# Performance work log

Hardware: AMD Instinct MI355X
Metric: run time of the kernel (lower is better)

## Reference

```python
import jax, jax.numpy as jnp
from jax import lax
import numpy as np

B, N, C = 8, 16384, 128
NPOINT, NSAMPLE = 1024, 64
RADIUS = 0.3
MLP = [C + 3, 64, 64, 128]  # use_xyz adds 3 input channels


def furthest_point_sample(xyz, npoint):
    """xyz: (B, N, 3) -> inds: (B, npoint) int32, iterative FPS starting at index 0."""
    b, n, _ = xyz.shape
    init_idx = jnp.zeros((b,), jnp.int32)
    mind0 = jnp.full((b, n), 1e10, xyz.dtype)

    def step(carry, _):
        mind, last = carry
        p = jnp.take_along_axis(xyz, last[:, None, None], axis=1)  # (B,1,3)
        d = jnp.sum((xyz - p) ** 2, axis=-1)                       # (B,N)
        mind = jnp.minimum(mind, d)
        nxt = jnp.argmax(mind, axis=-1).astype(jnp.int32)
        return (mind, nxt), nxt

    (_, _), rest = lax.scan(step, (mind0, init_idx), None, length=npoint - 1)
    return jnp.concatenate([init_idx[None], rest], axis=0).T  # (B, npoint)


def ball_query(xyz, new_xyz, radius, nsample):
    """Return (B, npoint, nsample) indices: first nsample points within radius of
    each center; slots past the found count are filled with the first in-ball index
    (matches CUDA ball_query semantics)."""
    n = xyz.shape[1]
    d2 = jnp.sum((new_xyz[:, :, None, :] - xyz[:, None, :, :]) ** 2, axis=-1)  # (B,npoint,N)
    mask = d2 < radius * radius
    score = jnp.where(mask, -jnp.arange(n, dtype=jnp.int32), jnp.int32(-n))
    top, _ = lax.top_k(score, nsample)            # largest scores = smallest valid indices
    idx = -top
    valid = top > -n
    return jnp.where(valid, idx, idx[..., :1])    # pad with first in-ball index


def gather_points(x, idx):
    """x: (B, N, D) or (B, D, N) gathered per batch along point axis via vmap."""
    if x.ndim == 3 and x.shape[-1] != idx.shape[-1]:
        pass
    return x


def reference(xyz, features, W0, b0, W1, b1, W2, b2):
    inds = furthest_point_sample(xyz, NPOINT)                               # (B,npoint)
    new_xyz = jax.vmap(lambda p, i: p[i])(xyz, inds)                        # (B,npoint,3)

    idx = ball_query(xyz, new_xyz, RADIUS, NSAMPLE)                         # (B,npoint,nsample)
    grouped_xyz = jax.vmap(lambda p, i: p[i])(xyz, idx)                     # (B,npoint,nsample,3)
    grouped_xyz = grouped_xyz - new_xyz[:, :, None, :]                      # center-relative
    gx = jnp.transpose(grouped_xyz, (0, 3, 1, 2))                           # (B,3,npoint,nsample)
    gf = jax.vmap(lambda f, i: f[:, i])(features, idx)                      # (B,C,npoint,nsample)
    x = jnp.concatenate([gx, gf], axis=1)                                   # (B,C+3,npoint,nsample)

    # SharedMLP: pointwise Conv2d (1x1) + ReLU per layer
    for W, b in ((W0, b0), (W1, b1), (W2, b2)):
        x = jax.nn.relu(jnp.einsum('bcps,oc->bops', x, W) + b[None, :, None, None])

    new_features = jnp.max(x, axis=-1)                                      # max pool over nsample
    return new_xyz, new_features, inds


def setup_inputs() -> dict:
    key = jax.random.key(0)
    ks = jax.random.split(key, 8)
    inp = {
        'xyz': jax.random.normal(ks[0], (B, N, 3), jnp.float32),
        'features': jax.random.normal(ks[1], (B, C, N), jnp.float32),
    }
    for i in range(3):
        cin, cout = MLP[i], MLP[i + 1]
        inp[f'W{i}'] = jax.random.normal(ks[2 + 2 * i], (cout, cin), jnp.float32) * 0.05
        inp[f'b{i}'] = jax.random.normal(ks[3 + 2 * i], (cout,), jnp.float32) * 0.01
    return inp
```

## Files before the change

kernel.cpp:

```cpp
#include <hip/hip_runtime.h>

#define BATCH   8
#define NPTS    16384
#define NCH     128
#define NPOINT  1024
#define NSAMPLE 64
#define CIN     131

#define THREADS  1024
#define FPS_PPT  (NPTS / THREADS)
#define CTAG     0x7C000000u

typedef unsigned long long u64;

__device__ __forceinline__ u64 u64max(u64 a, u64 b) { return a > b ? a : b; }

__device__ __forceinline__ u64 shfl_xor_u64(u64 v, int off) {
  const unsigned lo = __shfl_xor((unsigned)v, off, 64);
  const unsigned hi = __shfl_xor((unsigned)(v >> 32), off, 64);
  return ((u64)hi << 32) | lo;
}

__global__ void wtrans_kernel(const float* __restrict__ W0,
                              const float* __restrict__ W1,
                              const float* __restrict__ W2,
                              float* __restrict__ w0t,
                              float* __restrict__ w1t,
                              float* __restrict__ w2t)
{
  const int t = blockIdx.x * blockDim.x + threadIdx.x;
  if (t < 64 * CIN) { const int oc = t / CIN, ic = t % CIN; w0t[ic * 64  + oc] = W0[t]; }
  if (t < 64 * 64)  { const int oc = t >> 6,  ic = t & 63;  w1t[ic * 64  + oc] = W1[t]; }
  if (t < 128 * 64) { const int oc = t / 64,  ic = t % 64;  w2t[ic * 128 + oc] = W2[t]; }
}

__global__ __launch_bounds__(THREADS) void mega_kernel(
    const float* __restrict__ xyz, const float* __restrict__ feat,
    const float* __restrict__ w0t, const float* __restrict__ b0,
    const float* __restrict__ w1t, const float* __restrict__ b1,
    const float* __restrict__ w2t, const float* __restrict__ b2,
    float* __restrict__ out_newxyz, float* __restrict__ out_feat,
    float* __restrict__ out_inds_f, u64* __restrict__ cslot)
{
  __shared__ float sA[CIN * 64];
  __shared__ float sB[64 * 64];
  __shared__ int   s_idx[NSAMPLE];
  __shared__ int   bq[4][NSAMPLE];
  __shared__ int   bqcnt[4], bqfirst[4];
  __shared__ u64   s_w[2][16];
  __shared__ unsigned s_sel[4];

  const int t = threadIdx.x;

  if (blockIdx.x < BATCH) {
    const int b = blockIdx.x;
    const int lane = t & 63, wid = t >> 6;
    const float* __restrict__ p = xyz + (size_t)b * NPTS * 3;

    float xs[FPS_PPT], ys[FPS_PPT], zs[FPS_PPT], mind[FPS_PPT];
#pragma unroll
    for (int i = 0; i < FPS_PPT; ++i) {
      const int n = t + i * THREADS;
      xs[i] = p[n * 3 + 0];
      ys[i] = p[n * 3 + 1];
      zs[i] = p[n * 3 + 2];
      mind[i] = 1e10f;
    }

    u64* __restrict__ cs = cslot + (size_t)b * NPOINT * 4;

    float px = p[0], py = p[1], pz = p[2];
    if (t == 0) {
      out_inds_f[b * NPOINT] = 0.0f;
      const size_t o = (size_t)b * NPOINT * 3;
      out_newxyz[o + 0] = px; out_newxyz[o + 1] = py; out_newxyz[o + 2] = pz;
      const u64 tg = (u64)CTAG << 32;
      __hip_atomic_store(&cs[1], tg | __float_as_uint(px), __ATOMIC_RELAXED, __HIP_MEMORY_SCOPE_AGENT);
      __hip_atomic_store(&cs[2], tg | __float_as_uint(py), __ATOMIC_RELAXED, __HIP_MEMORY_SCOPE_AGENT);
      __hip_atomic_store(&cs[3], tg | __float_as_uint(pz), __ATOMIC_RELAXED, __HIP_MEMORY_SCOPE_AGENT);
      __hip_atomic_store(&cs[0], tg | 0u, __ATOMIC_RELAXED, __HIP_MEMORY_SCOPE_AGENT);
    }

    for (int k = 1; k < NPOINT; ++k) {
      const int par = k & 1;

      float bestv = -1.0f;
      int   besti = 0;
#pragma unroll
      for (int i = 0; i < FPS_PPT; ++i) {
        const float dx = xs[i] - px;
        const float dy = ys[i] - py;
        const float dz = zs[i] - pz;
        const float d = __fadd_rn(__fadd_rn(__fmul_rn(dx, dx), __fmul_rn(dy, dy)),
                                  __fmul_rn(dz, dz));
        const float m = fminf(mind[i], d);
        mind[i] = m;
        if (m > bestv) { bestv = m; besti = t + i * THREADS; }
      }

      u64 pk = ((u64)__float_as_uint(bestv) << 18) | (u64)(besti ^ 0x3FFFF);
#pragma unroll
      for (int off = 32; off >= 1; off >>= 1) pk = u64max(pk, shfl_xor_u64(pk, off));
      if (lane == 0) s_w[par][wid] = pk;
      __syncthreads();

      u64 bw = s_w[par][0];
#pragma unroll
      for (int i = 1; i < 16; ++i) bw = u64max(bw, s_w[par][i]);
      const int bi = (int)((~bw) & 0x3FFFF);

      px = p[bi * 3 + 0]; py = p[bi * 3 + 1]; pz = p[bi * 3 + 2];

      if (t == 0) {
        out_inds_f[b * NPOINT + k] = (float)bi;
        const size_t o = ((size_t)b * NPOINT + k) * 3;
        out_newxyz[o + 0] = px; out_newxyz[o + 1] = py; out_newxyz[o + 2] = pz;
        const u64 tg = (u64)(CTAG | (unsigned)k) << 32;
        u64* __restrict__ ck = cs + (size_t)k * 4;
        __hip_atomic_store(&ck[1], tg | __float_as_uint(px), __ATOMIC_RELAXED, __HIP_MEMORY_SCOPE_AGENT);
        __hip_atomic_store(&ck[2], tg | __float_as_uint(py), __ATOMIC_RELAXED, __HIP_MEMORY_SCOPE_AGENT);
        __hip_atomic_store(&ck[3], tg | __float_as_uint(pz), __ATOMIC_RELAXED, __HIP_MEMORY_SCOPE_AGENT);
        __hip_atomic_store(&ck[0], tg | (unsigned)bi, __ATOMIC_RELAXED, __HIP_MEMORY_SCOPE_AGENT);
      }
    }
    return;
  }

  const int c  = blockIdx.x - BATCH;
  const int b = c & 7, pc = c >> 3;
  const u64* __restrict__ cs = cslot + ((size_t)b * NPOINT + pc) * 4;

  if (t < 4) {
    const unsigned tg = CTAG | (unsigned)pc;
    u64 v;
    for (;;) {
      v = __hip_atomic_load(cs + t, __ATOMIC_RELAXED, __HIP_MEMORY_SCOPE_AGENT);
      if ((unsigned)(v >> 32) == tg) break;
      __builtin_amdgcn_s_sleep(8);
    }
    s_sel[t] = (unsigned)v;
  }
  __syncthreads();
  const float cx = __uint_as_float(s_sel[1]);
  const float cy = __uint_as_float(s_sel[2]);
  const float cz = __uint_as_float(s_sel[3]);
  const float* __restrict__ pb = xyz + (size_t)b * NPTS * 3;

  if (t < 256) {
    const int w = t >> 6, lane = t & 63;
    const float R2 = (float)(0.3 * 0.3);
    const int beg = w * (NPTS / 4);
    int cnt = 0, first = -1;
    for (int bs = beg; bs < beg + NPTS / 4; bs += 64) {
      const int n = bs + lane;
      const float dx = pb[n * 3 + 0] - cx;
      const float dy = pb[n * 3 + 1] - cy;
      const float dz = pb[n * 3 + 2] - cz;
      const float d = __fadd_rn(__fadd_rn(__fmul_rn(dx, dx), __fmul_rn(dy, dy)),
                                __fmul_rn(dz, dz));
      const bool in = d < R2;
      const u64 m = __ballot(in);
      if (first < 0 && m) first = bs + __ffsll(m) - 1;
      const int pos = __popcll(m & ((1ull << lane) - 1ull));
      if (in && cnt + pos < NSAMPLE) bq[w][cnt + pos] = n;
      cnt += __popcll(m);
      if (cnt >= NSAMPLE) break;
    }
    if (lane == 0) { bqcnt[w] = cnt < NSAMPLE ? cnt : NSAMPLE; bqfirst[w] = first; }
  }
  __syncthreads();
  if (t < NSAMPLE) {
    int firstAll = -1;
#pragma unroll
    for (int w = 0; w < 4; ++w)
      if (firstAll < 0 && bqfirst[w] >= 0) firstAll = bqfirst[w];
    int o = 0, val = -1;
#pragma unroll
    for (int w = 0; w < 4; ++w) {
      const int cw = bqcnt[w];
      if (val < 0 && t >= o && t < o + cw) val = bq[w][t - o];
      o += cw;
    }
    s_idx[t] = (val >= 0) ? val : firstAll;
  }
  __syncthreads();

  const int sm = t & 63, cg = t >> 6;
  const int is = s_idx[sm];
  if (cg == 0) {
    sA[0 * 64 + sm] = pb[is * 3 + 0] - cx;
    sA[1 * 64 + sm] = pb[is * 3 + 1] - cy;
    sA[2 * 64 + sm] = pb[is * 3 + 2] - cz;
  }
  const float* __restrict__ fb = feat + (size_t)b * NCH * NPTS;
  for (int ch = cg; ch < NCH; ch += 16)
    sA[(3 + ch) * 64 + sm] = fb[(size_t)ch * NPTS + is];
  __syncthreads();

  const int s0  = (t & 15) * 4;
  const int oc0 = ((t >> 4) & 15) * 4;

  if (t < 256) {
    float acc[4][4];
#pragma unroll
    for (int j = 0; j < 4; ++j) {
      const float bj = b0[oc0 + j];
#pragma unroll
      for (int i = 0; i < 4; ++i) acc[i][j] = bj;
    }
    for (int ic = 0; ic < CIN; ++ic) {
      const float4 xv = *(const float4*)&sA[ic * 64 + s0];
      const float4 wv = *(const float4*)&w0t[ic * 64 + oc0];
      const float xr[4] = {xv.x, xv.y, xv.z, xv.w};
      const float wr[4] = {wv.x, wv.y, wv.z, wv.w};
#pragma unroll
      for (int i = 0; i < 4; ++i)
#pragma unroll
        for (int j = 0; j < 4; ++j) acc[i][j] += xr[i] * wr[j];
    }
#pragma unroll
    for (int j = 0; j < 4; ++j) {
      float4 r;
      r.x = fmaxf(acc[0][j], 0.f); r.y = fmaxf(acc[1][j], 0.f);
      r.z = fmaxf(acc[2][j], 0.f); r.w = fmaxf(acc[3][j], 0.f);
      *(float4*)&sB[(oc0 + j) * 64 + s0] = r;
    }
  }
  __syncthreads();

  if (t < 256) {
    float acc[4][4];
#pragma unroll
    for (int j = 0; j < 4; ++j) {
      const float bj = b1[oc0 + j];
#pragma unroll
      for (int i = 0; i < 4; ++i) acc[i][j] = bj;
    }
    for (int ic = 0; ic < 64; ++ic) {
      const float4 xv = *(const float4*)&sB[ic * 64 + s0];
      const float4 wv = *(const float4*)&w1t[ic * 64 + oc0];
      const float xr[4] = {xv.x, xv.y, xv.z, xv.w};
      const float wr[4] = {wv.x, wv.y, wv.z, wv.w};
#pragma unroll
      for (int i = 0; i < 4; ++i)
#pragma unroll
        for (int j = 0; j < 4; ++j) acc[i][j] += xr[i] * wr[j];
    }
#pragma unroll
    for (int j = 0; j < 4; ++j) {
      float4 r;
      r.x = fmaxf(acc[0][j], 0.f); r.y = fmaxf(acc[1][j], 0.f);
      r.z = fmaxf(acc[2][j], 0.f); r.w = fmaxf(acc[3][j], 0.f);
      *(float4*)&sA[(oc0 + j) * 64 + s0] = r;
    }
  }
  __syncthreads();

  if (t < 256) {
    const int oc8 = ((t >> 4) & 15) * 8;
    float acc[4][8];
#pragma unroll
    for (int j = 0; j < 8; ++j) {
      const float bj = b2[oc8 + j];
#pragma unroll
      for (int i = 0; i < 4; ++i) acc[i][j] = bj;
    }
    for (int ic = 0; ic < 64; ++ic) {
      const float4 xv  = *(const float4*)&sA[ic * 64 + s0];
      const float4 wlo = *(const float4*)&w2t[ic * 128 + oc8];
      const float4 whi = *(const float4*)&w2t[ic * 128 + oc8 + 4];
      const float xr[4] = {xv.x, xv.y, xv.z, xv.w};
      const float wr[8] = {wlo.x, wlo.y, wlo.z, wlo.w, whi.x, whi.y, whi.z, whi.w};
#pragma unroll
      for (int i = 0; i < 4; ++i)
#pragma unroll
        for (int j = 0; j < 8; ++j) acc[i][j] += xr[i] * wr[j];
    }
    float m[8];
#pragma unroll
    for (int j = 0; j < 8; ++j)
      m[j] = fmaxf(fmaxf(acc[0][j], acc[1][j]), fmaxf(acc[2][j], acc[3][j]));
#pragma unroll
    for (int off = 8; off >= 1; off >>= 1) {
#pragma unroll
      for (int j = 0; j < 8; ++j)
        m[j] = fmaxf(m[j], __shfl_xor(m[j], off, 64));
    }
    if ((t & 15) == 0) {
#pragma unroll
      for (int j = 0; j < 8; ++j)
        out_feat[((size_t)b * NCH + oc8 + j) * NPOINT + pc] = fmaxf(m[j], 0.f);
    }
  }
}

extern "C" void kernel_launch(void* const* d_in, const int* in_sizes, int n_in,
                              void* d_out, int out_size, void* d_ws, size_t ws_size,
                              hipStream_t stream)
{
  const float* xyz  = (const float*)d_in[0];
  const float* feat = (const float*)d_in[1];
  const float* W0   = (const float*)d_in[2];
  const float* b0   = (const float*)d_in[3];
  const float* W1   = (const float*)d_in[4];
  const float* b1   = (const float*)d_in[5];
  const float* W2   = (const float*)d_in[6];
  const float* b2   = (const float*)d_in[7];

  float* out_newxyz = (float*)d_out;
  float* out_feat   = out_newxyz + (size_t)BATCH * NPOINT * 3;
  float* out_inds_f = out_feat + (size_t)BATCH * NCH * NPOINT;

  char* ws = (char*)d_ws;
  u64* cslot = (u64*)ws;
  float* w0t = (float*)(ws + 262144);
  float* w1t = w0t + 64 * CIN;
  float* w2t = w1t + 64 * 64;

  hipMemsetAsync(cslot, 0, 262144, stream);
  wtrans_kernel<<<dim3((64 * CIN + 255) / 256), dim3(256), 0, stream>>>(
      W0, W1, W2, w0t, w1t, w2t);
  mega_kernel<<<dim3(BATCH + BATCH * NPOINT), dim3(THREADS), 0, stream>>>(
      xyz, feat, w0t, b0, w1t, b1, w2t, b2,
      out_newxyz, out_feat, out_inds_f, cslot);
}
```

Before: 2.025 ms.

## Morton-sort points so FPS threads skip distance updates via bounding-box pruning

Adds a per-batch kernel that computes Morton codes on a 16^3 grid and bitonic-sorts the points in shared memory, so each FPS thread owns 16 spatially adjacent points. Each FPS thread keeps a bounding box and its current max of min-distances. It skips the distance update when the new centre's box lower bound cannot reduce any of its distances, and reuses its cached candidate. This is meant to cut the per-iteration ALU work of the serial FPS loop, which dominates the runtime. The cost is an extra sort launch, gathered (non-coalesced) point loads, tie-breaking by original index to keep results exact, and a pruning threshold that depends on a floating-point slack factor.

```diff
diff --git a/kernel.cpp b/kernel.cpp
--- a/kernel.cpp
+++ b/kernel.cpp
@@ -8,7 +8,7 @@
 #define CIN     131
 
 #define THREADS  1024
-#define FPS_PPT  (NPTS / THREADS)
+#define TPP      16
 #define CTAG     0x7C000000u
 
 typedef unsigned long long u64;
@@ -19,6 +19,104 @@
   const unsigned lo = __shfl_xor((unsigned)v, off, 64);
   const unsigned hi = __shfl_xor((unsigned)(v >> 32), off, 64);
   return ((u64)hi << 32) | lo;
+}
+
+__global__ __launch_bounds__(1024) void sort_kernel(
+    const float* __restrict__ xyz, int* __restrict__ sorig)
+{
+  const int b = blockIdx.x, t = threadIdx.x;
+  const float* __restrict__ p = xyz + (size_t)b * NPTS * 3;
+  __shared__ unsigned keys[NPTS];
+
+  float lx[16], ly[16], lz[16];
+  float mnx = 1e30f, mxx = -1e30f, mny = 1e30f, mxy = -1e30f;
+  float mnz = 1e30f, mxz = -1e30f;
+#pragma unroll
+  for (int i = 0; i < 16; ++i) {
+    const int n = t + i * 1024;
+    lx[i] = p[n * 3 + 0]; ly[i] = p[n * 3 + 1]; lz[i] = p[n * 3 + 2];
+    mnx = fminf(mnx, lx[i]); mxx = fmaxf(mxx, lx[i]);
+    mny = fminf(mny, ly[i]); mxy = fmaxf(mxy, ly[i]);
+    mnz = fminf(mnz, lz[i]); mxz = fmaxf(mxz, lz[i]);
+  }
+#pragma unroll
+  for (int off = 32; off >= 1; off >>= 1) {
+    mnx = fminf(mnx, __shfl_xor(mnx, off, 64)); mxx = fmaxf(mxx, __shfl_xor(mxx, off, 64));
+    mny = fminf(mny, __shfl_xor(mny, off, 64)); mxy = fmaxf(mxy, __shfl_xor(mxy, off, 64));
+    mnz = fminf(mnz, __shfl_xor(mnz, off, 64)); mxz = fmaxf(mxz, __shfl_xor(mxz, off, 64));
+  }
+  if ((t & 63) == 0) {
+    const int w = t >> 6;
+    keys[w * 6 + 0] = __float_as_uint(mnx); keys[w * 6 + 1] = __float_as_uint(mxx);
+    keys[w * 6 + 2] = __float_as_uint(mny); keys[w * 6 + 3] = __float_as_uint(mxy);
+    keys[w * 6 + 4] = __float_as_uint(mnz); keys[w * 6 + 5] = __float_as_uint(mxz);
+  }
+  __syncthreads();
+  if (t == 0) {
+    float a0 = __uint_as_float(keys[0]), a1 = __uint_as_float(keys[1]);
+    float a2 = __uint_as_float(keys[2]), a3 = __uint_as_float(keys[3]);
+    float a4 = __uint_as_float(keys[4]), a5 = __uint_as_float(keys[5]);
+    for (int w = 1; w < 16; ++w) {
+      a0 = fminf(a0, __uint_as_float(keys[w * 6 + 0]));
+      a1 = fmaxf(a1, __uint_as_float(keys[w * 6 + 1]));
+      a2 = fminf(a2, __uint_as_float(keys[w * 6 + 2]));
+      a3 = fmaxf(a3, __uint_as_float(keys[w * 6 + 3]));
+      a4 = fminf(a4, __uint_as_float(keys[w * 6 + 4]));
+      a5 = fmaxf(a5, __uint_as_float(keys[w * 6 + 5]));
+    }
+    keys[0] = __float_as_uint(a0); keys[1] = __float_as_uint(a1);
+    keys[2] = __float_as_uint(a2); keys[3] = __float_as_uint(a3);
+    keys[4] = __float_as_uint(a4); keys[5] = __float_as_uint(a5);
+  }
+  __syncthreads();
+  const float bnx = __uint_as_float(keys[0]);
+  const float bxx = __uint_as_float(keys[1]);
+  const float bny = __uint_as_float(keys[2]);
+  const float bxy = __uint_as_float(keys[3]);
+  const float bnz = __uint_as_float(keys[4]);
+  const float bxz = __uint_as_float(keys[5]);
+  __syncthreads();
+
+  const float ivx = 15.9999f / fmaxf(bxx - bnx, 1e-20f);
+  const float ivy = 15.9999f / fmaxf(bxy - bny, 1e-20f);
+  const float ivz = 15.9999f / fmaxf(bxz - bnz, 1e-20f);
+#pragma unroll
+  for (int i = 0; i < 16; ++i) {
+    const int n = t + i * 1024;
+    int cx = (int)((lx[i] - bnx) * ivx);
+    int cy = (int)((ly[i] - bny) * ivy);
+    int cz = (int)((lz[i] - bnz) * ivz);
+    cx = min(15, max(0, cx)); cy = min(15, max(0, cy)); cz = min(15, max(0, cz));
+    unsigned m = 0;
+#pragma unroll
+    for (int j = 0; j < 4; ++j)
+      m |= (((unsigned)(cx >> j) & 1u) << (3 * j))
+         | (((unsigned)(cy >> j) & 1u) << (3 * j + 1))
+         | (((unsigned)(cz >> j) & 1u) << (3 * j + 2));
+    keys[n] = (m << 14) | (unsigned)n;
+  }
+  __syncthreads();
+
+  for (unsigned kk = 2; kk <= (unsigned)NPTS; kk <<= 1) {
+    for (unsigned j = kk >> 1; j > 0; j >>= 1) {
+#pragma unroll
+      for (int w = 0; w < 16; ++w) {
+        const unsigned i = (unsigned)t + (unsigned)w * 1024u;
+        const unsigned l = i ^ j;
+        if (l > i) {
+          const unsigned a = keys[i], c = keys[l];
+          const bool asc = ((i & kk) == 0);
+          if ((a > c) == asc) { keys[i] = c; keys[l] = a; }
+        }
+      }
+      __syncthreads();
+    }
+  }
+
+  for (int i = 0; i < 16; ++i) {
+    const int pos = t + i * 1024;
+    sorig[(size_t)b * NPTS + pos] = (int)(keys[pos] & 0x3FFFu);
+  }
 }
 
 __global__ void wtrans_kernel(const float* __restrict__ W0,
@@ -36,6 +134,7 @@
 
 __global__ __launch_bounds__(THREADS) void mega_kernel(
     const float* __restrict__ xyz, const float* __restrict__ feat,
+    const int* __restrict__ sorig,
     const float* __restrict__ w0t, const float* __restrict__ b0,
     const float* __restrict__ w1t, const float* __restrict__ b1,
     const float* __restrict__ w2t, const float* __restrict__ b2,
@@ -56,16 +155,28 @@
     const int b = blockIdx.x;
     const int lane = t & 63, wid = t >> 6;
     const float* __restrict__ p = xyz + (size_t)b * NPTS * 3;
-
-    float xs[FPS_PPT], ys[FPS_PPT], zs[FPS_PPT], mind[FPS_PPT];
-#pragma unroll
-    for (int i = 0; i < FPS_PPT; ++i) {
-      const int n = t + i * THREADS;
-      xs[i] = p[n * 3 + 0];
-      ys[i] = p[n * 3 + 1];
-      zs[i] = p[n * 3 + 2];
+    const int* __restrict__ so = sorig + (size_t)b * NPTS;
+
+    int   oid[TPP];
+    float xs[TPP], ys[TPP], zs[TPP], mind[TPP];
+#pragma unroll
+    for (int i = 0; i < TPP; ++i) oid[i] = so[t * TPP + i];
+#pragma unroll
+    for (int i = 0; i < TPP; ++i) {
+      const int n = oid[i];
+      xs[i] = p[n * 3 + 0]; ys[i] = p[n * 3 + 1]; zs[i] = p[n * 3 + 2];
       mind[i] = 1e10f;
     }
+    float lox = xs[0], hix = xs[0], loy = ys[0], hiy = ys[0], loz = zs[0], hiz = zs[0];
+#pragma unroll
+    for (int i = 1; i < TPP; ++i) {
+      lox = fminf(lox, xs[i]); hix = fmaxf(hix, xs[i]);
+      loy = fminf(loy, ys[i]); hiy = fmaxf(hiy, ys[i]);
+      loz = fminf(loz, zs[i]); hiz = fmaxf(hiz, zs[i]);
+    }
+
+    u64   cpk  = 0;
+    float tmax = 1e10f;
 
     u64* __restrict__ cs = cslot + (size_t)b * NPOINT * 4;
 
@@ -84,21 +195,35 @@
     for (int k = 1; k < NPOINT; ++k) {
       const int par = k & 1;
 
-      float bestv = -1.0f;
-      int   besti = 0;
-#pragma unroll
-      for (int i = 0; i < FPS_PPT; ++i) {
-        const float dx = xs[i] - px;
-        const float dy = ys[i] - py;
-        const float dz = zs[i] - pz;
-        const float d = __fadd_rn(__fadd_rn(__fmul_rn(dx, dx), __fmul_rn(dy, dy)),
-                                  __fmul_rn(dz, dz));
-        const float m = fminf(mind[i], d);
-        mind[i] = m;
-        if (m > bestv) { bestv = m; besti = t + i * THREADS; }
+      const float ux = fmaxf(fmaxf(lox - px, px - hix), 0.f);
+      const float uy = fmaxf(fmaxf(loy - py, py - hiy), 0.f);
+      const float uz = fmaxf(fmaxf(loz - pz, pz - hiz), 0.f);
+      const float lb = ux * ux + uy * uy + uz * uz;
+      const bool need = (lb * 0.999996f < tmax);
+
+      if (__ballot(need) != 0ull) {
+        if (need) {
+          float bestv = -1.0f;
+          int   boid  = 0x7FFFFFFF;
+#pragma unroll
+          for (int i = 0; i < TPP; ++i) {
+            const float dx = xs[i] - px;
+            const float dy = ys[i] - py;
+            const float dz = zs[i] - pz;
+            const float d = __fadd_rn(__fadd_rn(__fmul_rn(dx, dx), __fmul_rn(dy, dy)),
+                                      __fmul_rn(dz, dz));
+            const float m = fminf(mind[i], d);
+            mind[i] = m;
+            const bool c = (m > bestv) || (m == bestv && oid[i] < boid);
+            bestv = c ? m : bestv;
+            boid  = c ? oid[i] : boid;
+          }
+          tmax = bestv;
+          cpk  = ((u64)__float_as_uint(bestv) << 14) | (u64)(boid ^ 0x3FFF);
+        }
       }
 
-      u64 pk = ((u64)__float_as_uint(bestv) << 18) | (u64)(besti ^ 0x3FFFF);
+      u64 pk = cpk;
 #pragma unroll
       for (int off = 32; off >= 1; off >>= 1) pk = u64max(pk, shfl_xor_u64(pk, off));
       if (lane == 0) s_w[par][wid] = pk;
@@ -107,7 +232,7 @@
       u64 bw = s_w[par][0];
 #pragma unroll
       for (int i = 1; i < 16; ++i) bw = u64max(bw, s_w[par][i]);
-      const int bi = (int)((~bw) & 0x3FFFF);
+      const int bi = (int)((bw & 0x3FFF) ^ 0x3FFF);
 
       px = p[bi * 3 + 0]; py = p[bi * 3 + 1]; pz = p[bi * 3 + 2];
 
@@ -313,14 +438,16 @@
 
   char* ws = (char*)d_ws;
   u64* cslot = (u64*)ws;
-  float* w0t = (float*)(ws + 262144);
+  int* sorig = (int*)(ws + 262144);
+  float* w0t = (float*)(ws + 262144 + 524288);
   float* w1t = w0t + 64 * CIN;
   float* w2t = w1t + 64 * 64;
 
   hipMemsetAsync(cslot, 0, 262144, stream);
   wtrans_kernel<<<dim3((64 * CIN + 255) / 256), dim3(256), 0, stream>>>(
       W0, W1, W2, w0t, w1t, w2t);
+  sort_kernel<<<dim3(BATCH), dim3(1024), 0, stream>>>(xyz, sorig);
   mega_kernel<<<dim3(BATCH + BATCH * NPOINT), dim3(THREADS), 0, stream>>>(
-      xyz, feat, w0t, b0, w1t, b1, w2t, b2,
+      xyz, feat, sorig, w0t, b0, w1t, b1, w2t, b2,
       out_newxyz, out_feat, out_inds_f, cslot);
 }
```

Measured after the change: 2.198 ms. 8.6% more time.

## Pass FPS winner coordinates through LDS instead of reloading from global memory

Applied to the files above, without the earlier changes.

Each thread now tracks the coordinates of its local farthest point. The wave winner, identified by a wave id packed into the low bits of the key, writes those coordinates to shared memory, so the next center comes from LDS rather than a dependent global load on every FPS iteration. The 16-way block reduction becomes a balanced tree, and the index field shrinks to 14 bits to make room for the wave id. A large dummy LDS pad is also allocated and touched, apparently to cap blocks per CU so consumer blocks do not crowd the FPS blocks, at the cost of lower occupancy for the grouping/MLP blocks.

```diff
diff --git a/kernel.cpp b/kernel.cpp
--- a/kernel.cpp
+++ b/kernel.cpp
@@ -8,7 +8,7 @@
 #define CIN     131
 
 #define THREADS  1024
-#define FPS_PPT  (NPTS / THREADS)
+#define TPP      (NPTS / THREADS)
 #define CTAG     0x7C000000u
 
 typedef unsigned long long u64;
@@ -48,18 +48,21 @@
   __shared__ int   bq[4][NSAMPLE];
   __shared__ int   bqcnt[4], bqfirst[4];
   __shared__ u64   s_w[2][16];
+  __shared__ unsigned s_c[2][16][3];
   __shared__ unsigned s_sel[4];
+  __shared__ u64   lds_pad[3800];
 
   const int t = threadIdx.x;
+  { volatile u64* vp = lds_pad; vp[t] = (u64)t; }
 
   if (blockIdx.x < BATCH) {
     const int b = blockIdx.x;
     const int lane = t & 63, wid = t >> 6;
     const float* __restrict__ p = xyz + (size_t)b * NPTS * 3;
 
-    float xs[FPS_PPT], ys[FPS_PPT], zs[FPS_PPT], mind[FPS_PPT];
-#pragma unroll
-    for (int i = 0; i < FPS_PPT; ++i) {
+    float xs[TPP], ys[TPP], zs[TPP], mind[TPP];
+#pragma unroll
+    for (int i = 0; i < TPP; ++i) {
       const int n = t + i * THREADS;
       xs[i] = p[n * 3 + 0];
       ys[i] = p[n * 3 + 1];
@@ -86,8 +89,9 @@
 
       float bestv = -1.0f;
       int   besti = 0;
-#pragma unroll
-      for (int i = 0; i < FPS_PPT; ++i) {
+      float bx = 0.f, by = 0.f, bz = 0.f;
+#pragma unroll
+      for (int i = 0; i < TPP; ++i) {
         const float dx = xs[i] - px;
         const float dy = ys[i] - py;
         const float dz = zs[i] - pz;
@@ -95,21 +99,42 @@
                                   __fmul_rn(dz, dz));
         const float m = fminf(mind[i], d);
         mind[i] = m;
-        if (m > bestv) { bestv = m; besti = t + i * THREADS; }
+        if (m > bestv) { bestv = m; besti = t + i * THREADS;
+                         bx = xs[i]; by = ys[i]; bz = zs[i]; }
       }
 
-      u64 pk = ((u64)__float_as_uint(bestv) << 18) | (u64)(besti ^ 0x3FFFF);
+      const u64 pk0 = ((u64)__float_as_uint(bestv) << 18)
+                    | ((u64)(besti ^ 0x3FFF) << 4) | (u64)wid;
+      u64 pk = pk0;
 #pragma unroll
       for (int off = 32; off >= 1; off >>= 1) pk = u64max(pk, shfl_xor_u64(pk, off));
-      if (lane == 0) s_w[par][wid] = pk;
+
+      if (pk == pk0) {
+        s_w[par][wid] = pk;
+        s_c[par][wid][0] = __float_as_uint(bx);
+        s_c[par][wid][1] = __float_as_uint(by);
+        s_c[par][wid][2] = __float_as_uint(bz);
+      }
       __syncthreads();
 
-      u64 bw = s_w[par][0];
-#pragma unroll
-      for (int i = 1; i < 16; ++i) bw = u64max(bw, s_w[par][i]);
-      const int bi = (int)((~bw) & 0x3FFFF);
-
-      px = p[bi * 3 + 0]; py = p[bi * 3 + 1]; pz = p[bi * 3 + 2];
+      u64 a0 = u64max(s_w[par][0],  s_w[par][1]);
+      u64 a1 = u64max(s_w[par][2],  s_w[par][3]);
+      u64 a2 = u64max(s_w[par][4],  s_w[par][5]);
+      u64 a3 = u64max(s_w[par][6],  s_w[par][7]);
+      u64 a4 = u64max(s_w[par][8],  s_w[par][9]);
+      u64 a5 = u64max(s_w[par][10], s_w[par][11]);
+      u64 a6 = u64max(s_w[par][12], s_w[par][13]);
+      u64 a7 = u64max(s_w[par][14], s_w[par][15]);
+      a0 = u64max(a0, a1); a2 = u64max(a2, a3);
+      a4 = u64max(a4, a5); a6 = u64max(a6, a7);
+      a0 = u64max(a0, a2); a4 = u64max(a4, a6);
+      const u64 bw = u64max(a0, a4);
+
+      const int slot = (int)(bw & 15);
+      const int bi   = (int)(((bw >> 4) & 0x3FFF) ^ 0x3FFF);
+      px = __uint_as_float(s_c[par][slot][0]);
+      py = __uint_as_float(s_c[par][slot][1]);
+      pz = __uint_as_float(s_c[par][slot][2]);
 
       if (t == 0) {
         out_inds_f[b * NPOINT + k] = (float)bi;
```

After: 2.580 ms. 1.27x slower.
